# Performance work log

Hardware: AMD Instinct MI355X
Metric: run time of the kernel (lower is better)

Reference implementation:

```python
import jax, jax.numpy as jnp
import numpy as np

D = 128      # d_model
H = 4        # heads == edge embedding dim
C = D // H   # per-head channels
L = 4        # gnn layers
N = 200000   # batched atoms
E = 400000   # batched directed bonds
G = 8000     # molecules in batch
NTASK = 1
NEG_SLOPE = 0.2


def setup_inputs() -> dict:
    key = jax.random.key(0)
    ks = jax.random.split(key, 12)
    s = 0.05
    x = jax.random.randint(ks[0], (N, 9), 0, 16)            # atom features
    edge_index = jax.random.randint(ks[1], (2, E), 0, N)    # [src; dst]
    edge_attr = jax.random.randint(ks[2], (E,), 0, 10)      # bond types
    batch_ids = jnp.sort(jax.random.randint(ks[3], (N,), 0, G))
    atom_tables = jax.random.normal(ks[4], (9, 16, D), jnp.float32) * s
    bond_table = jax.random.normal(ks[5], (10, H), jnp.float32) * s
    Wl = jax.random.normal(ks[6], (L, D, D), jnp.float32) * s   # lin_l per layer
    bl = jnp.zeros((L, D), jnp.float32)
    Wr = jax.random.normal(ks[7], (L, D, D), jnp.float32) * s   # lin_r per layer
    br = jnp.zeros((L, D), jnp.float32)
    We = jax.random.normal(ks[8], (L, H, D), jnp.float32) * s   # lin_edge (no bias)
    att = jax.random.normal(ks[9], (L, H, C), jnp.float32) * s  # attention vector a
    cb = jnp.zeros((L, D), jnp.float32)                          # conv output bias
    Wout = jax.random.normal(ks[10], (D, NTASK), jnp.float32) * s
    bout = jnp.zeros((NTASK,), jnp.float32)
    return dict(atom_tables=atom_tables, bond_table=bond_table, Wl=Wl, bl=bl,
                Wr=Wr, br=br, We=We, att=att, cb=cb, Wout=Wout, bout=bout,
                x=x, edge_index=edge_index, edge_attr=edge_attr, batch_ids=batch_ids)


def _segment_softmax(logits, seg, num_segments):
    # logits: [Ef, H], softmax over edges sharing the same target node
    m = jax.ops.segment_max(logits, seg, num_segments=num_segments)
    e = jnp.exp(logits - m[seg])
    z = jax.ops.segment_sum(e, seg, num_segments=num_segments)
    return e / (z[seg] + 1e-16)


def _forward(atom_tables, bond_table, Wl, bl, Wr, br, We, att, cb, Wout, bout,
             x, edge_index, edge_attr, batch_ids):
    # Atom encoder: sum of per-feature embeddings -> [N, D]
    h = atom_tables[jnp.arange(9)[None, :], x].sum(axis=1)
    # Bond encoder -> [E, H]
    e_emb = bond_table[edge_attr]
    src, dst = edge_index[0], edge_index[1]
    n = h.shape[0]
    # add_self_loops with fill_value='mean': per-target mean of incoming edge feats
    sums = jax.ops.segment_sum(e_emb, dst, num_segments=n)
    cnt = jax.ops.segment_sum(jnp.ones((e_emb.shape[0],), e_emb.dtype), dst,
                              num_segments=n)
    loop_attr = sums / jnp.maximum(cnt, 1.0)[:, None]
    ar = jnp.arange(n)
    src_f = jnp.concatenate([src, ar])
    dst_f = jnp.concatenate([dst, ar])
    e_full = jnp.concatenate([e_emb, loop_attr], axis=0)   # [E+N, H]

    for l in range(L):
        xl = (h @ Wl[l] + bl[l]).reshape(n, H, C)
        xr = (h @ Wr[l] + br[l]).reshape(n, H, C)
        ee = (e_full @ We[l]).reshape(-1, H, C)            # [E+N, H, C]
        g = jax.nn.leaky_relu(xl[src_f] + xr[dst_f] + ee, NEG_SLOPE)
        logits = jnp.einsum('ehc,hc->eh', g, att[l])
        alpha = _segment_softmax(logits, dst_f, n)         # [E+N, H]
        out = jax.ops.segment_sum(xl[src_f] * alpha[:, :, None], dst_f,
                                  num_segments=n)
        h = out.reshape(n, D) + cb[l]
        if l < L - 1:
            h = jax.nn.relu(h)

    # global add pool over molecules, then linear head
    pooled = jax.ops.segment_sum(h, batch_ids, num_segments=G)  # [G, D]
    return pooled @ Wout + bout                                  # [G, num_tasks]


def reference(atom_tables, bond_table, Wl, bl, Wr, br, We, att, cb, Wout, bout,
              x, edge_index, edge_attr, batch_ids):
    return _forward(atom_tables, bond_table, Wl, bl, Wr, br, We, att, cb, Wout,
                    bout, x, edge_index, edge_attr, batch_ids)
```

## Files before the change

### kernel.cpp

```cpp
#include <hip/hip_runtime.h>
#include <hip/hip_bf16.h>

#define DD 128
#define NHEAD 4
#define CHAN 32
#define NEG 0.2f

typedef short bf16x8 __attribute__((ext_vector_type(8)));
typedef float f32x4 __attribute__((ext_vector_type(4)));

__device__ inline ushort f2bf(float x) {
  unsigned u = __float_as_uint(x);
  return (ushort)((u + 0x7FFF + ((u >> 16) & 1)) >> 16);
}

__global__ void k_atom_enc(const int* __restrict__ x, const float* __restrict__ tab,
                           float* __restrict__ h, int N) {
  int idx = blockIdx.x * blockDim.x + threadIdx.x;
  if (idx >= N * DD) return;
  int n = idx >> 7, d = idx & 127;
  const int* xr = x + n * 9;
  float s = 0.f;
#pragma unroll
  for (int f = 0; f < 9; f++) {
    int v = xr[f];
    s += tab[(f * 16 + v) * DD + d];
  }
  h[idx] = s;
}

__global__ void k_init(int* __restrict__ deg, float* __restrict__ cnt,
                       float* __restrict__ sums, int N) {
  int i = blockIdx.x * blockDim.x + threadIdx.x;
  if (i >= N) return;
  deg[i] = 1;
  cnt[i] = 0.f;
  sums[i * 4 + 0] = 0.f; sums[i * 4 + 1] = 0.f;
  sums[i * 4 + 2] = 0.f; sums[i * 4 + 3] = 0.f;
}

__global__ void k_edge_count(const int* __restrict__ ei, const int* __restrict__ eattr,
                             const float* __restrict__ btab, float* __restrict__ e_emb,
                             float* __restrict__ sums, float* __restrict__ cnt,
                             int* __restrict__ deg, int E) {
  int e = blockIdx.x * blockDim.x + threadIdx.x;
  if (e >= E) return;
  int d = ei[E + e];
  int a = eattr[e];
  float f0 = btab[a * 4 + 0], f1 = btab[a * 4 + 1];
  float f2 = btab[a * 4 + 2], f3 = btab[a * 4 + 3];
  e_emb[e * 4 + 0] = f0; e_emb[e * 4 + 1] = f1;
  e_emb[e * 4 + 2] = f2; e_emb[e * 4 + 3] = f3;
  atomicAdd(&sums[d * 4 + 0], f0);
  atomicAdd(&sums[d * 4 + 1], f1);
  atomicAdd(&sums[d * 4 + 2], f2);
  atomicAdd(&sums[d * 4 + 3], f3);
  atomicAdd(&cnt[d], 1.0f);
  atomicAdd(&deg[d], 1);
}

__global__ void k_loopattr(float* __restrict__ sums, const float* __restrict__ cnt, int N) {
  int i = blockIdx.x * blockDim.x + threadIdx.x;
  if (i >= N * 4) return;
  sums[i] = sums[i] / fmaxf(cnt[i >> 2], 1.0f);
}

__global__ void k_scan_block(const int* __restrict__ deg, int* __restrict__ bsums, int N) {
  __shared__ int sh[256];
  int t = threadIdx.x;
  int base = blockIdx.x * 2048 + t * 8;
  int tot = 0;
#pragma unroll
  for (int i = 0; i < 8; i++) tot += (base + i < N) ? deg[base + i] : 0;
  sh[t] = tot;
  __syncthreads();
  for (int off = 128; off > 0; off >>= 1) {
    if (t < off) sh[t] += sh[t + off];
    __syncthreads();
  }
  if (t == 0) bsums[blockIdx.x] = sh[0];
}

__global__ void k_scan_top(int* __restrict__ bsums, int* __restrict__ rowptr,
                           int nblk, int N) {
  if (threadIdx.x == 0 && blockIdx.x == 0) {
    int run = 0;
    for (int b = 0; b < nblk; b++) { int v = bsums[b]; bsums[b] = run; run += v; }
    rowptr[N] = run;
  }
}

__global__ void k_scan_down(const int* __restrict__ deg, const int* __restrict__ bsums,
                            int* __restrict__ rowptr, int* __restrict__ cursor, int N) {
  __shared__ int sh[256];
  int t = threadIdx.x;
  int base = blockIdx.x * 2048 + t * 8;
  int v[8]; int tot = 0;
#pragma unroll
  for (int i = 0; i < 8; i++) { v[i] = (base + i < N) ? deg[base + i] : 0; tot += v[i]; }
  sh[t] = tot;
  __syncthreads();
  for (int off = 1; off < 256; off <<= 1) {
    int xv = (t >= off) ? sh[t - off] : 0;
    __syncthreads();
    sh[t] += xv;
    __syncthreads();
  }
  int run = bsums[blockIdx.x] + sh[t] - tot;
#pragma unroll
  for (int i = 0; i < 8; i++) {
    if (base + i < N) { rowptr[base + i] = run; cursor[base + i] = run; run += v[i]; }
  }
}

__global__ void k_scatter(const int* __restrict__ ei, int* __restrict__ cursor,
                          int* __restrict__ eid, int E, int N) {
  int t = blockIdx.x * blockDim.x + threadIdx.x;
  if (t >= E + N) return;
  int d = (t < E) ? ei[E + t] : (t - E);
  int pos = atomicAdd(&cursor[d], 1);
  eid[pos] = t;
}

__global__ void k_wpack(const float* __restrict__ Wl, const float* __restrict__ Wr,
                        ushort* __restrict__ Bhi, ushort* __restrict__ Blo, int L) {
  int tid = blockIdx.x * blockDim.x + threadIdx.x;
  int total = L * 2 * 4 * 8 * 64;
  if (tid >= total) return;
  int lane = tid & 63;
  int nt = (tid >> 6) & 7;
  int kb = (tid >> 9) & 3;
  int mat = (tid >> 11) & 1;
  int layer = tid >> 12;
  const float* W = (mat ? Wr : Wl) + (size_t)layer * DD * DD;
  int kbase = kb * 32 + (lane >> 4) * 8;
  int n = nt * 16 + (lane & 15);
  size_t out = (size_t)(layer * 2 + mat) * 16384 +
               ((size_t)(kb * 8 + nt) * 64 + lane) * 8;
#pragma unroll
  for (int j = 0; j < 8; j++) {
    float xv = W[(size_t)(kbase + j) * DD + n];
    ushort h_ = f2bf(xv);
    float fh = __uint_as_float((unsigned)h_ << 16);
    ushort l_ = f2bf(xv - fh);
    Bhi[out + j] = h_;
    Blo[out + j] = l_;
  }
}

__global__ __launch_bounds__(256) void k_gemm2_mfma(const float* h,
    const ushort* __restrict__ bhiL, const ushort* __restrict__ bloL,
    const ushort* __restrict__ bhiR, const ushort* __restrict__ bloR,
    const float* __restrict__ bl, const float* __restrict__ br,
    float* xl, float* xr, int N) {
  __shared__ ushort sAhi[64 * 128];
  __shared__ ushort sAlo[64 * 128];
  int t = threadIdx.x;
  int A0 = blockIdx.x * 64;
  {
    int a = t >> 2;
    int kq = (t & 3) * 32;
    int n = A0 + a;
    const float* hp = &h[(size_t)n * DD + kq];
    int swz = (a & 7) << 4;
    int rowb = a * 256;
#pragma unroll
    for (int i = 0; i < 8; i++) {
      float4 v = (n < N) ? *(const float4*)(hp + i * 4) : make_float4(0, 0, 0, 0);
      float fv[4] = {v.x, v.y, v.z, v.w};
      ushort hiw[4], low[4];
#pragma unroll
      for (int j = 0; j < 4; j++) {
        ushort h_ = f2bf(fv[j]);
        float fh = __uint_as_float((unsigned)h_ << 16);
        hiw[j] = h_;
        low[j] = f2bf(fv[j] - fh);
      }
      int inrow = (kq + i * 4) * 2;
      int off = rowb + (inrow ^ swz);
      *(ushort4*)((char*)sAhi + off) = make_ushort4(hiw[0], hiw[1], hiw[2], hiw[3]);
      *(ushort4*)((char*)sAlo + off) = make_ushort4(low[0], low[1], low[2], low[3]);
    }
  }
  __syncthreads();

  int lane = t & 63;
  int w = t >> 6;
  int arow = lane & 15;
  int acol = (lane >> 4) * 16;
  int swzr = (arow & 7) << 4;

  f32x4 accL[4][2], accR[4][2];
#pragma unroll
  for (int mt = 0; mt < 4; mt++)
#pragma unroll
    for (int nti = 0; nti < 2; nti++) {
      accL[mt][nti] = (f32x4){0.f, 0.f, 0.f, 0.f};
      accR[mt][nti] = (f32x4){0.f, 0.f, 0.f, 0.f};
    }

  for (int kb = 0; kb < 4; kb++) {
    bf16x8 ahi[4], alo[4];
#pragma unroll
    for (int mt = 0; mt < 4; mt++) {
      int abyte = (mt * 16 + arow) * 256 + ((kb * 64 + acol) ^ swzr);
      ahi[mt] = *(const bf16x8*)((const char*)sAhi + abyte);
      alo[mt] = *(const bf16x8*)((const char*)sAlo + abyte);
    }
#pragma unroll
    for (int nti = 0; nti < 2; nti++) {
      int nt = w * 2 + nti;
      size_t fo = ((size_t)(kb * 8 + nt) * 64 + lane) * 8;
      bf16x8 bhl = *(const bf16x8*)(bhiL + fo);
      bf16x8 bll = *(const bf16x8*)(bloL + fo);
      bf16x8 bhr = *(const bf16x8*)(bhiR + fo);
      bf16x8 blr = *(const bf16x8*)(bloR + fo);
#pragma unroll
      for (int mt = 0; mt < 4; mt++) {
        accL[mt][nti] = __builtin_amdgcn_mfma_f32_16x16x32_bf16(ahi[mt], bhl, accL[mt][nti], 0, 0, 0);
        accR[mt][nti] = __builtin_amdgcn_mfma_f32_16x16x32_bf16(ahi[mt], bhr, accR[mt][nti], 0, 0, 0);
        accL[mt][nti] = __builtin_amdgcn_mfma_f32_16x16x32_bf16(ahi[mt], bll, accL[mt][nti], 0, 0, 0);
        accR[mt][nti] = __builtin_amdgcn_mfma_f32_16x16x32_bf16(ahi[mt], blr, accR[mt][nti], 0, 0, 0);
        accL[mt][nti] = __builtin_amdgcn_mfma_f32_16x16x32_bf16(alo[mt], bhl, accL[mt][nti], 0, 0, 0);
        accR[mt][nti] = __builtin_amdgcn_mfma_f32_16x16x32_bf16(alo[mt], bhr, accR[mt][nti], 0, 0, 0);
      }
    }
  }

  int col = lane & 15;
  int rgrp = (lane >> 4) * 4;
#pragma unroll
  for (int nti = 0; nti < 2; nti++) {
    int n = (w * 2 + nti) * 16 + col;
    float bLv = bl[n], bRv = br[n];
#pragma unroll
    for (int mt = 0; mt < 4; mt++) {
#pragma unroll
      for (int r = 0; r < 4; r++) {
        int atom = A0 + mt * 16 + rgrp + r;
        if (atom < N) {
          xl[(size_t)atom * DD + n] = accL[mt][nti][r] + bLv;
          xr[(size_t)atom * DD + n] = accR[mt][nti][r] + bRv;
        }
      }
    }
  }
}

__global__ __launch_bounds__(256) void k_attn(
    const float* __restrict__ xl, const float* xr,
    const float* __restrict__ e_emb, const float* __restrict__ la,
    const int* __restrict__ ei, const int* __restrict__ rowptr,
    const int* __restrict__ eid,
    const float* __restrict__ Wep, const float* __restrict__ attp,
    const float* __restrict__ cbp,
    const float* __restrict__ Woutp, const int* __restrict__ bid,
    float* __restrict__ outp,
    float* hout, int N, int E, int flags) {
  int wid = threadIdx.x >> 6;
  int lane = threadIdx.x & 63;
  int n = blockIdx.x * 4 + wid;
  if (n >= N) return;
  int d0 = lane * 2;
  float we0[4], we1[4];
#pragma unroll
  for (int j = 0; j < 4; j++) {
    we0[j] = Wep[j * DD + d0];
    we1[j] = Wep[j * DD + d0 + 1];
  }
  int hh = lane >> 4;
  float a0 = attp[hh * 32 + (d0 & 31)];
  float a1 = attp[hh * 32 + ((d0 + 1) & 31)];
  float2 xr2 = *(const float2*)&xr[(size_t)n * DD + d0];
  float m = -3.0e38f, z = 0.f, acc0 = 0.f, acc1 = 0.f;
  int r0 = rowptr[n], r1 = rowptr[n + 1];
  for (int p0 = r0; p0 < r1; p0 += 4) {
    int nb = r1 - p0; nb = nb > 4 ? 4 : nb;
    int ss[4]; float4 ff[4]; float2 xv[4];
#pragma unroll
    for (int j = 0; j < 4; j++) {
      int p = p0 + j; p = (p < r1) ? p : (r1 - 1);
      int e = eid[p];
      bool re = e < E;
      ss[j] = re ? ei[e] : n;
      ff[j] = re ? *(const float4*)&e_emb[(size_t)e * 4]
                 : *(const float4*)&la[(size_t)n * 4];
    }
#pragma unroll
    for (int j = 0; j < 4; j++)
      xv[j] = *(const float2*)&xl[(size_t)ss[j] * DD + d0];
#pragma unroll
    for (int j = 0; j < 4; j++) {
      if (j < nb) {
        float ee0 = ff[j].x * we0[0] + ff[j].y * we0[1] + ff[j].z * we0[2] + ff[j].w * we0[3];
        float ee1 = ff[j].x * we1[0] + ff[j].y * we1[1] + ff[j].z * we1[2] + ff[j].w * we1[3];
        float g0 = xv[j].x + xr2.x + ee0; g0 = g0 > 0.f ? g0 : NEG * g0;
        float g1 = xv[j].y + xr2.y + ee1; g1 = g1 > 0.f ? g1 : NEG * g1;
        float pv = g0 * a0 + g1 * a1;
        pv += __shfl_xor(pv, 1);
        pv += __shfl_xor(pv, 2);
        pv += __shfl_xor(pv, 4);
        pv += __shfl_xor(pv, 8);
        float mn = fmaxf(m, pv);
        float sc = __expf(m - mn);
        float w  = __expf(pv - mn);
        z = z * sc + w;
        acc0 = acc0 * sc + w * xv[j].x;
        acc1 = acc1 * sc + w * xv[j].y;
        m = mn;
      }
    }
  }
  float inv = 1.f / (z + 1e-16f);
  float o0 = acc0 * inv + cbp[d0];
  float o1 = acc1 * inv + cbp[d0 + 1];
  if (flags & 1) { o0 = fmaxf(o0, 0.f); o1 = fmaxf(o1, 0.f); }
  if (flags & 2) {
    float v = o0 * Woutp[d0] + o1 * Woutp[d0 + 1];
    v += __shfl_xor(v, 1);
    v += __shfl_xor(v, 2);
    v += __shfl_xor(v, 4);
    v += __shfl_xor(v, 8);
    v += __shfl_xor(v, 16);
    v += __shfl_xor(v, 32);
    if (lane == 0) atomicAdd(&outp[bid[n]], v);
  } else {
    *(float2*)&hout[(size_t)n * DD + d0] = make_float2(o0, o1);
  }
}

__global__ void k_head_init(float* __restrict__ out, const float* __restrict__ bout, int G) {
  int i = blockIdx.x * blockDim.x + threadIdx.x;
  if (i < G) out[i] = bout[0];
}

extern "C" void kernel_launch(void* const* d_in, const int* in_sizes, int n_in,
                              void* d_out, int out_size, void* d_ws, size_t ws_size,
                              hipStream_t stream) {
  const float* atom_tables = (const float*)d_in[0];
  const float* bond_table  = (const float*)d_in[1];
  const float* Wl   = (const float*)d_in[2];
  const float* bl   = (const float*)d_in[3];
  const float* Wr   = (const float*)d_in[4];
  const float* br   = (const float*)d_in[5];
  const float* We   = (const float*)d_in[6];
  const float* att  = (const float*)d_in[7];
  const float* cb   = (const float*)d_in[8];
  const float* Wout = (const float*)d_in[9];
  const float* bout = (const float*)d_in[10];
  const int* x      = (const int*)d_in[11];
  const int* ei     = (const int*)d_in[12];
  const int* eattr  = (const int*)d_in[13];
  const int* bid    = (const int*)d_in[14];

  int N = in_sizes[11] / 9;
  int E = in_sizes[13];
  int G = out_size;
  int L = in_sizes[3] / DD;

  char* p = (char*)d_ws;
  auto alloc = [&](size_t bytes) {
    char* r = p;
    p += (bytes + 255) & ~(size_t)255;
    return r;
  };
  float* hx     = (float*)alloc((size_t)N * DD * 4);
  float* xl     = (float*)alloc((size_t)N * DD * 4);
  float* e_emb  = (float*)alloc((size_t)E * 4 * 4);
  float* sums   = (float*)alloc((size_t)N * 4 * 4);
  int*   rowptr = (int*)alloc((size_t)(N + 1) * 4);
  int*   eid    = (int*)alloc((size_t)(E + N) * 4);
  float* cnt    = (float*)alloc((size_t)N * 4);
  int*   deg    = (int*)alloc((size_t)N * 4);
  int*   cursor = (int*)alloc((size_t)N * 4);
  int nblk = (N + 2047) / 2048;
  int*   bsums  = (int*)alloc((size_t)nblk * 4);
  ushort* Bhi   = (ushort*)alloc((size_t)L * 2 * 16384 * 2);
  ushort* Blo   = (ushort*)alloc((size_t)L * 2 * 16384 * 2);
  float* out    = (float*)d_out;

  if ((size_t)(p - (char*)d_ws) > ws_size) return;

  hipLaunchKernelGGL(k_atom_enc, dim3((N * DD + 255) / 256), dim3(256), 0, stream,
                     x, atom_tables, hx, N);
  hipLaunchKernelGGL(k_init, dim3((N + 255) / 256), dim3(256), 0, stream,
                     deg, cnt, sums, N);
  hipLaunchKernelGGL(k_edge_count, dim3((E + 255) / 256), dim3(256), 0, stream,
                     ei, eattr, bond_table, e_emb, sums, cnt, deg, E);
  hipLaunchKernelGGL(k_scan_block, dim3(nblk), dim3(256), 0, stream, deg, bsums, N);
  hipLaunchKernelGGL(k_scan_top, dim3(1), dim3(64), 0, stream, bsums, rowptr, nblk, N);
  hipLaunchKernelGGL(k_scan_down, dim3(nblk), dim3(256), 0, stream,
                     deg, bsums, rowptr, cursor, N);
  hipLaunchKernelGGL(k_scatter, dim3((E + N + 255) / 256), dim3(256), 0, stream,
                     ei, cursor, eid, E, N);
  hipLaunchKernelGGL(k_loopattr, dim3((N * 4 + 255) / 256), dim3(256), 0, stream,
                     sums, cnt, N);
  {
    int total = L * 2 * 4 * 8 * 64;
    hipLaunchKernelGGL(k_wpack, dim3((total + 255) / 256), dim3(256), 0, stream,
                       Wl, Wr, Bhi, Blo, L);
  }
  hipLaunchKernelGGL(k_head_init, dim3((G + 255) / 256), dim3(256), 0, stream,
                     out, bout, G);

  for (int l = 0; l < L; l++) {
    const ushort* bhiL = Bhi + (size_t)(l * 2 + 0) * 16384;
    const ushort* bhiR = Bhi + (size_t)(l * 2 + 1) * 16384;
    const ushort* bloL = Blo + (size_t)(l * 2 + 0) * 16384;
    const ushort* bloR = Blo + (size_t)(l * 2 + 1) * 16384;
    hipLaunchKernelGGL(k_gemm2_mfma, dim3((N + 63) / 64), dim3(256), 0, stream,
                       hx, bhiL, bloL, bhiR, bloR,
                       bl + (size_t)l * DD, br + (size_t)l * DD, xl, hx, N);
    int flags = (l < L - 1) ? 1 : 2;
    hipLaunchKernelGGL(k_attn, dim3((N + 3) / 4), dim3(256), 0, stream,
                       xl, hx, e_emb, sums, ei, rowptr, eid,
                       We + (size_t)l * NHEAD * DD, att + (size_t)l * NHEAD * CHAN,
                       cb + (size_t)l * DD, Wout, bid, out, hx, N, E, flags);
  }
}
```

Baseline: 1.265 ms.

## Store xl/xr projections in bf16 and batch per-block head atomics

The GEMM kernel now writes the lin_l and lin_r projections as bf16 instead of fp32. xl goes to its own half-size buffer, and xr is packed into the first half of each hx row, which is reused in place. This halves the bytes of the random per-edge gather of xl rows and of the xr reads in the attention kernel. The attention loop is reorganised to batch the four edge logits before the shuffle reductions and to use a multiplicative mask in place of the branch. The final-layer pooling combines atomics from consecutive nodes of the same molecule within a block, at the cost of a __syncthreads. Rounding xl and xr to bf16 reduces accuracy compared with the earlier hi/lo split-precision GEMM.

```diff
diff --git a/kernel.cpp b/kernel.cpp
--- a/kernel.cpp
+++ b/kernel.cpp
@@ -12,6 +12,9 @@
 __device__ inline ushort f2bf(float x) {
   unsigned u = __float_as_uint(x);
   return (ushort)((u + 0x7FFF + ((u >> 16) & 1)) >> 16);
+}
+__device__ inline float bf2f(ushort u) {
+  return __uint_as_float((unsigned)u << 16);
 }
 
 __global__ void k_atom_enc(const int* __restrict__ x, const float* __restrict__ tab,
@@ -152,7 +155,7 @@
     const ushort* __restrict__ bhiL, const ushort* __restrict__ bloL,
     const ushort* __restrict__ bhiR, const ushort* __restrict__ bloR,
     const float* __restrict__ bl, const float* __restrict__ br,
-    float* xl, float* xr, int N) {
+    ushort* __restrict__ xlb, float* xr_rows, int N) {
   __shared__ ushort sAhi[64 * 128];
   __shared__ ushort sAlo[64 * 128];
   int t = threadIdx.x;
@@ -227,6 +230,7 @@
     }
   }
 
+  ushort* xru = (ushort*)xr_rows;
   int col = lane & 15;
   int rgrp = (lane >> 4) * 4;
 #pragma unroll
@@ -239,8 +243,8 @@
       for (int r = 0; r < 4; r++) {
         int atom = A0 + mt * 16 + rgrp + r;
         if (atom < N) {
-          xl[(size_t)atom * DD + n] = accL[mt][nti][r] + bLv;
-          xr[(size_t)atom * DD + n] = accR[mt][nti][r] + bRv;
+          xlb[(size_t)atom * DD + n]  = f2bf(accL[mt][nti][r] + bLv);
+          xru[(size_t)atom * 256 + n] = f2bf(accR[mt][nti][r] + bRv);
         }
       }
     }
@@ -248,7 +252,7 @@
 }
 
 __global__ __launch_bounds__(256) void k_attn(
-    const float* __restrict__ xl, const float* xr,
+    const ushort* __restrict__ xlb, const float* xr_rows,
     const float* __restrict__ e_emb, const float* __restrict__ la,
     const int* __restrict__ ei, const int* __restrict__ rowptr,
     const int* __restrict__ eid,
@@ -257,64 +261,81 @@
     const float* __restrict__ Woutp, const int* __restrict__ bid,
     float* __restrict__ outp,
     float* hout, int N, int E, int flags) {
+  __shared__ float sv[4];
+  __shared__ int   sb[4];
   int wid = threadIdx.x >> 6;
   int lane = threadIdx.x & 63;
   int n = blockIdx.x * 4 + wid;
-  if (n >= N) return;
+  bool act = n < N;
   int d0 = lane * 2;
-  float we0[4], we1[4];
-#pragma unroll
-  for (int j = 0; j < 4; j++) {
-    we0[j] = Wep[j * DD + d0];
-    we1[j] = Wep[j * DD + d0 + 1];
-  }
-  int hh = lane >> 4;
-  float a0 = attp[hh * 32 + (d0 & 31)];
-  float a1 = attp[hh * 32 + ((d0 + 1) & 31)];
-  float2 xr2 = *(const float2*)&xr[(size_t)n * DD + d0];
-  float m = -3.0e38f, z = 0.f, acc0 = 0.f, acc1 = 0.f;
-  int r0 = rowptr[n], r1 = rowptr[n + 1];
-  for (int p0 = r0; p0 < r1; p0 += 4) {
-    int nb = r1 - p0; nb = nb > 4 ? 4 : nb;
-    int ss[4]; float4 ff[4]; float2 xv[4];
+  float o0 = 0.f, o1 = 0.f;
+  if (act) {
+    float we0[4], we1[4];
 #pragma unroll
     for (int j = 0; j < 4; j++) {
-      int p = p0 + j; p = (p < r1) ? p : (r1 - 1);
-      int e = eid[p];
-      bool re = e < E;
-      ss[j] = re ? ei[e] : n;
-      ff[j] = re ? *(const float4*)&e_emb[(size_t)e * 4]
-                 : *(const float4*)&la[(size_t)n * 4];
-    }
-#pragma unroll
-    for (int j = 0; j < 4; j++)
-      xv[j] = *(const float2*)&xl[(size_t)ss[j] * DD + d0];
-#pragma unroll
-    for (int j = 0; j < 4; j++) {
-      if (j < nb) {
+      we0[j] = Wep[j * DD + d0];
+      we1[j] = Wep[j * DD + d0 + 1];
+    }
+    int hh = lane >> 4;
+    float a0 = attp[hh * 32 + (d0 & 31)];
+    float a1 = attp[hh * 32 + ((d0 + 1) & 31)];
+    const ushort* xru = (const ushort*)xr_rows;
+    ushort2 xru2 = *(const ushort2*)&xru[(size_t)n * 256 + d0];
+    float xr0 = bf2f(xru2.x), xr1 = bf2f(xru2.y);
+    float4 la4 = *(const float4*)&la[(size_t)n * 4];
+    float m = -3.0e38f, z = 0.f, acc0 = 0.f, acc1 = 0.f;
+    int r0 = rowptr[n], r1 = rowptr[n + 1];
+    for (int p0 = r0; p0 < r1; p0 += 4) {
+      int ss[4]; float4 ff[4];
+      float xv0[4], xv1[4], pv[4];
+#pragma unroll
+      for (int j = 0; j < 4; j++) {
+        int p = p0 + j; p = (p < r1) ? p : (r1 - 1);
+        int e = eid[p];
+        bool re = e < E;
+        ss[j] = re ? ei[e] : n;
+        ff[j] = re ? *(const float4*)&e_emb[(size_t)e * 4] : la4;
+      }
+#pragma unroll
+      for (int j = 0; j < 4; j++) {
+        ushort2 u = *(const ushort2*)&xlb[(size_t)ss[j] * DD + d0];
+        xv0[j] = bf2f(u.x); xv1[j] = bf2f(u.y);
+      }
+#pragma unroll
+      for (int j = 0; j < 4; j++) {
         float ee0 = ff[j].x * we0[0] + ff[j].y * we0[1] + ff[j].z * we0[2] + ff[j].w * we0[3];
         float ee1 = ff[j].x * we1[0] + ff[j].y * we1[1] + ff[j].z * we1[2] + ff[j].w * we1[3];
-        float g0 = xv[j].x + xr2.x + ee0; g0 = g0 > 0.f ? g0 : NEG * g0;
-        float g1 = xv[j].y + xr2.y + ee1; g1 = g1 > 0.f ? g1 : NEG * g1;
-        float pv = g0 * a0 + g1 * a1;
-        pv += __shfl_xor(pv, 1);
-        pv += __shfl_xor(pv, 2);
-        pv += __shfl_xor(pv, 4);
-        pv += __shfl_xor(pv, 8);
-        float mn = fmaxf(m, pv);
+        float g0 = xv0[j] + xr0 + ee0; g0 = g0 > 0.f ? g0 : NEG * g0;
+        float g1 = xv1[j] + xr1 + ee1; g1 = g1 > 0.f ? g1 : NEG * g1;
+        pv[j] = g0 * a0 + g1 * a1;
+      }
+#pragma unroll
+      for (int j = 0; j < 4; j++) {
+        pv[j] += __shfl_xor(pv[j], 1);
+        pv[j] += __shfl_xor(pv[j], 2);
+        pv[j] += __shfl_xor(pv[j], 4);
+        pv[j] += __shfl_xor(pv[j], 8);
+      }
+#pragma unroll
+      for (int j = 0; j < 4; j++) {
+        float msk = (p0 + j < r1) ? 1.f : 0.f;
+        float mn = fmaxf(m, pv[j]);
         float sc = __expf(m - mn);
-        float w  = __expf(pv - mn);
-        z = z * sc + w;
-        acc0 = acc0 * sc + w * xv[j].x;
-        acc1 = acc1 * sc + w * xv[j].y;
+        float wj = __expf(pv[j] - mn) * msk;
+        z = z * sc + wj;
+        acc0 = acc0 * sc + wj * xv0[j];
+        acc1 = acc1 * sc + wj * xv1[j];
         m = mn;
       }
     }
-  }
-  float inv = 1.f / (z + 1e-16f);
-  float o0 = acc0 * inv + cbp[d0];
-  float o1 = acc1 * inv + cbp[d0 + 1];
-  if (flags & 1) { o0 = fmaxf(o0, 0.f); o1 = fmaxf(o1, 0.f); }
+    float inv = 1.f / (z + 1e-16f);
+    o0 = acc0 * inv + cbp[d0];
+    o1 = acc1 * inv + cbp[d0 + 1];
+    if (flags & 1) { o0 = fmaxf(o0, 0.f); o1 = fmaxf(o1, 0.f); }
+    if (!(flags & 2)) {
+      *(float2*)&hout[(size_t)n * DD + d0] = make_float2(o0, o1);
+    }
+  }
   if (flags & 2) {
     float v = o0 * Woutp[d0] + o1 * Woutp[d0 + 1];
     v += __shfl_xor(v, 1);
@@ -323,9 +344,23 @@
     v += __shfl_xor(v, 8);
     v += __shfl_xor(v, 16);
     v += __shfl_xor(v, 32);
-    if (lane == 0) atomicAdd(&outp[bid[n]], v);
-  } else {
-    *(float2*)&hout[(size_t)n * DD + d0] = make_float2(o0, o1);
+    if (lane == 0) {
+      sv[wid] = v;
+      sb[wid] = act ? bid[n] : -1;
+    }
+    __syncthreads();
+    if (threadIdx.x == 0) {
+      int i = 0;
+      while (i < 4) {
+        int b = sb[i];
+        if (b < 0) { i++; continue; }
+        float s = sv[i];
+        int j = i + 1;
+        while (j < 4 && sb[j] == b) { s += sv[j]; j++; }
+        atomicAdd(&outp[b], s);
+        i = j;
+      }
+    }
   }
 }
 
@@ -364,20 +399,20 @@
     p += (bytes + 255) & ~(size_t)255;
     return r;
   };
-  float* hx     = (float*)alloc((size_t)N * DD * 4);
-  float* xl     = (float*)alloc((size_t)N * DD * 4);
-  float* e_emb  = (float*)alloc((size_t)E * 4 * 4);
-  float* sums   = (float*)alloc((size_t)N * 4 * 4);
-  int*   rowptr = (int*)alloc((size_t)(N + 1) * 4);
-  int*   eid    = (int*)alloc((size_t)(E + N) * 4);
-  float* cnt    = (float*)alloc((size_t)N * 4);
-  int*   deg    = (int*)alloc((size_t)N * 4);
-  int*   cursor = (int*)alloc((size_t)N * 4);
+  float*  hx     = (float*)alloc((size_t)N * DD * 4);
+  ushort* xlb    = (ushort*)alloc((size_t)N * DD * 2);
+  float*  e_emb  = (float*)alloc((size_t)E * 4 * 4);
+  float*  sums   = (float*)alloc((size_t)N * 4 * 4);
+  int*    rowptr = (int*)alloc((size_t)(N + 1) * 4);
+  int*    eid    = (int*)alloc((size_t)(E + N) * 4);
+  float*  cnt    = (float*)alloc((size_t)N * 4);
+  int*    deg    = (int*)alloc((size_t)N * 4);
+  int*    cursor = (int*)alloc((size_t)N * 4);
   int nblk = (N + 2047) / 2048;
-  int*   bsums  = (int*)alloc((size_t)nblk * 4);
-  ushort* Bhi   = (ushort*)alloc((size_t)L * 2 * 16384 * 2);
-  ushort* Blo   = (ushort*)alloc((size_t)L * 2 * 16384 * 2);
-  float* out    = (float*)d_out;
+  int*    bsums  = (int*)alloc((size_t)nblk * 4);
+  ushort* Bhi    = (ushort*)alloc((size_t)L * 2 * 16384 * 2);
+  ushort* Blo    = (ushort*)alloc((size_t)L * 2 * 16384 * 2);
+  float*  out    = (float*)d_out;
 
   if ((size_t)(p - (char*)d_ws) > ws_size) return;
 
@@ -410,10 +445,10 @@
     const ushort* bloR = Blo + (size_t)(l * 2 + 1) * 16384;
     hipLaunchKernelGGL(k_gemm2_mfma, dim3((N + 63) / 64), dim3(256), 0, stream,
                        hx, bhiL, bloL, bhiR, bloR,
-                       bl + (size_t)l * DD, br + (size_t)l * DD, xl, hx, N);
+                       bl + (size_t)l * DD, br + (size_t)l * DD, xlb, hx, N);
     int flags = (l < L - 1) ? 1 : 2;
     hipLaunchKernelGGL(k_attn, dim3((N + 3) / 4), dim3(256), 0, stream,
-                       xl, hx, e_emb, sums, ei, rowptr, eid,
+                       xlb, hx, e_emb, sums, ei, rowptr, eid,
                        We + (size_t)l * NHEAD * DD, att + (size_t)l * NHEAD * CHAN,
                        cb + (size_t)l * DD, Wout, bid, out, hx, N, E, flags);
   }
```

Measured after the change: 1.231 ms. 2.6% less time.
